# Performance work log

Hardware: AMD Instinct MI355X
Metric: run time of the kernel (lower is better)

## Reference

```python
import jax, jax.numpy as jnp
import numpy as np

D_MODEL, D_STATE, D_CONV, EXPAND = 1024, 16, 4, 2
D_INNER = EXPAND * D_MODEL
DT_RANK = (D_MODEL + 15) // 16  # 64
B_SZ, SEQ = 2, 1024


def _mamba_dir(x, inW, convW, convB, xpW, dtW, dtB, Alog, Dp, outW):
    """Standard Mamba block forward. x: [B, L, d_model]."""
    Bsz, L, _ = x.shape
    d_inner, d_state = Alog.shape
    dt_rank = xpW.shape[0] - 2 * d_state
    xz = jnp.einsum('bld,ed->ble', x, inW)            # [B, L, 2*d_inner]
    xi, z = jnp.split(xz, 2, axis=-1)
    # depthwise causal conv along L
    xc = jnp.swapaxes(xi, 1, 2)                       # [B, d_inner, L]
    xc = jax.lax.conv_general_dilated(
        xc, convW, window_strides=(1,),
        padding=[(convW.shape[-1] - 1, 0)],
        feature_group_count=d_inner)
    xc = xc + convB[None, :, None]
    u = jax.nn.silu(jnp.swapaxes(xc, 1, 2))           # [B, L, d_inner]
    x_dbl = jnp.einsum('bld,ed->ble', u, xpW)         # [B, L, dt_rank+2N]
    dt, Bm, Cm = jnp.split(x_dbl, [dt_rank, dt_rank + d_state], axis=-1)
    delta = jax.nn.softplus(jnp.einsum('blr,dr->bld', dt, dtW) + dtB)  # [B,L,d_inner]
    A = -jnp.exp(Alog)                                # [d_inner, d_state]

    def step(h, ins):
        d_t, B_t, C_t, u_t = ins                      # [B,D],[B,N],[B,N],[B,D]
        dA = jnp.exp(d_t[:, :, None] * A)             # [B, D, N]
        h = h * dA + (d_t * u_t)[:, :, None] * B_t[:, None, :]
        y_t = jnp.einsum('bdn,bn->bd', h, C_t)
        return h, y_t

    h0 = jnp.zeros((Bsz, d_inner, d_state), x.dtype)
    xs = (jnp.swapaxes(delta, 0, 1), jnp.swapaxes(Bm, 0, 1),
          jnp.swapaxes(Cm, 0, 1), jnp.swapaxes(u, 0, 1))
    _, ys = jax.lax.scan(step, h0, xs)
    y = jnp.swapaxes(ys, 0, 1)                        # [B, L, d_inner]
    y = y + u * Dp
    y = y * jax.nn.silu(z)
    return jnp.einsum('bld,od->blo', y, outW)         # [B, L, d_model]


def _make_params(key, suffix):
    ks = jax.random.split(key, 10)
    s = 0.02
    p = {
        'inW' + suffix: jax.random.normal(ks[0], (2 * D_INNER, D_MODEL), jnp.float32) * s,
        'convW' + suffix: jax.random.normal(ks[1], (D_INNER, 1, D_CONV), jnp.float32) * s,
        'convB' + suffix: jnp.zeros((D_INNER,), jnp.float32),
        'xpW' + suffix: jax.random.normal(ks[2], (DT_RANK + 2 * D_STATE, D_INNER), jnp.float32) * s,
        'dtW' + suffix: jax.random.normal(ks[3], (D_INNER, DT_RANK), jnp.float32) * s,
        'dtB' + suffix: jax.random.normal(ks[4], (D_INNER,), jnp.float32) * 0.1 - 4.0,
        'Alog' + suffix: jnp.log(1.0 + jax.random.uniform(ks[5], (D_INNER, D_STATE), jnp.float32) * 15.0),
        'Dp' + suffix: jnp.ones((D_INNER,), jnp.float32),
        'outW' + suffix: jax.random.normal(ks[6], (D_MODEL, D_INNER), jnp.float32) * s,
    }
    return p


def setup_inputs() -> dict:
    key = jax.random.key(0)
    kx, kf, kb = jax.random.split(key, 3)
    inp = {'x': jax.random.normal(kx, (B_SZ, SEQ, D_MODEL), jnp.float32)}
    inp.update(_make_params(kf, '_f'))
    inp.update(_make_params(kb, '_b'))
    return inp


def reference(x, inW_f, convW_f, convB_f, xpW_f, dtW_f, dtB_f, Alog_f, Dp_f, outW_f,
              inW_b, convW_b, convB_b, xpW_b, dtW_b, dtB_b, Alog_b, Dp_b, outW_b):
    y_fwd = _mamba_dir(x, inW_f, convW_f, convB_f, xpW_f, dtW_f, dtB_f, Alog_f, Dp_f, outW_f)
    xb = jnp.flip(x, axis=1)
    y_bwd = jnp.flip(_mamba_dir(xb, inW_b, convW_b, convB_b, xpW_b, dtW_b, dtB_b, Alog_b, Dp_b, outW_b), axis=1)
    return 0.5 * (y_fwd + y_bwd)
```

## Files before the change

kernel.cpp:

```cpp
#include <hip/hip_runtime.h>
#include <math.h>

#define B_SZ 2
#define SEQ  1024
#define DM   1024
#define DI   2048
#define NST  16
#define RNK  64
#define XPD  96
#define M_TOT (B_SZ*SEQ)
#define NC   32
#define LC   (SEQ/NC)
#define NCH  65536

typedef unsigned short ushort_t;
typedef __attribute__((ext_vector_type(8))) short short8;
typedef __attribute__((ext_vector_type(4))) float f32x4;

#if __has_builtin(__builtin_amdgcn_exp2f)
#define EXP2F __builtin_amdgcn_exp2f
#else
#define EXP2F exp2f
#endif
#define LOG2E 1.44269504f

__device__ __forceinline__ ushort_t f2bf(float f) {
    unsigned u = __float_as_uint(f);
    u += 0x7fff + ((u >> 16) & 1);
    return (ushort_t)(u >> 16);
}
__device__ __forceinline__ float bf2f(ushort_t v) {
    return __uint_as_float(((unsigned)v) << 16);
}

__global__ __launch_bounds__(256)
void convert_all(const float* __restrict__ x,
                 const float* __restrict__ inWf, const float* __restrict__ inWb,
                 const float* __restrict__ outWf, const float* __restrict__ outWb,
                 const float* __restrict__ xpWf, const float* __restrict__ xpWb,
                 ushort_t* __restrict__ xbf, ushort_t* __restrict__ inWcat,
                 ushort_t* __restrict__ outWcat, ushort_t* __restrict__ xpWcat)
{
    int bid = blockIdx.x;
    const float* src; ushort_t* dst; int rel; int strided = 0;
    if (bid < 2048)       { rel = bid;         src = x;     dst = xbf; }
    else if (bid < 6144)  { rel = bid - 2048;  src = inWf;  dst = inWcat; }
    else if (bid < 10240) { rel = bid - 6144;  src = inWb;  dst = inWcat + (size_t)2 * DI * DM; }
    else if (bid < 12288) { rel = bid - 10240; src = outWf; dst = outWcat;      strided = 1; }
    else if (bid < 14336) { rel = bid - 12288; src = outWb; dst = outWcat + DI; strided = 1; }
    else if (bid < 14528) { rel = bid - 14336; src = xpWf;  dst = xpWcat; }
    else                  { rel = bid - 14528; src = xpWb;  dst = xpWcat + (size_t)XPD * DI; }
    int i = rel * 256 + threadIdx.x;
    float4 v = ((const float4*)src)[i];
    ushort4 o;
    o.x = f2bf(v.x); o.y = f2bf(v.y); o.z = f2bf(v.z); o.w = f2bf(v.w);
    if (!strided) {
        ((ushort4*)dst)[i] = o;
    } else {
        int row = i >> 9;
        int c4  = (i - (row << 9)) << 2;
        *(ushort4*)(dst + (size_t)row * (2 * DI) + c4) = o;
    }
}

__device__ __forceinline__ void load_lds16(const ushort_t* g, ushort_t* l) {
    __builtin_amdgcn_global_load_lds(
        (const __attribute__((address_space(1))) void*)g,
        (__attribute__((address_space(3))) void*)l, 16, 0, 0);
}

template<bool OUT_BF16>
__global__ __launch_bounds__(256)
void gemm_gll(const ushort_t* __restrict__ A, const ushort_t* __restrict__ W,
              void* __restrict__ D, int M, int N, int K, int kLen, int ldD)
{
    __shared__ __align__(16) ushort_t As[128 * 64];
    __shared__ __align__(16) ushort_t Ws[128 * 64];
    const int t    = threadIdx.x;
    const int lane = t & 63;
    const int wave = t >> 6;
    const int wr   = (wave >> 1) * 64;
    const int wc   = (wave & 1) * 64;

    const int m0 = blockIdx.y * 128;
    const int n0 = blockIdx.x * 128;
    const int kStart = blockIdx.z * kLen;

    const int srow   = lane >> 3;
    const int gchunk = (lane & 7) ^ srow;

    f32x4 acc[4][4] = {};

    for (int k0 = kStart; k0 < kStart + kLen; k0 += 64) {
#pragma unroll
        for (int it = 0; it < 4; it++) {
            const int rb = wave * 32 + it * 8;
            load_lds16(A + (size_t)(m0 + rb + srow) * K + k0 + gchunk * 8,
                       As + rb * 64);
            load_lds16(W + (size_t)(n0 + rb + srow) * K + k0 + gchunk * 8,
                       Ws + rb * 64);
        }
        __syncthreads();
#pragma unroll
        for (int kk = 0; kk < 2; kk++) {
            const int kc = kk * 4 + (lane >> 4);
            short8 af[4], bf[4];
#pragma unroll
            for (int i = 0; i < 4; i++) {
                int r = wr + i * 16 + (lane & 15);
                af[i] = *(const short8*)(As + r * 64 + ((kc ^ (r & 7)) << 3));
            }
#pragma unroll
            for (int j = 0; j < 4; j++) {
                int r = wc + j * 16 + (lane & 15);
                bf[j] = *(const short8*)(Ws + r * 64 + ((kc ^ (r & 7)) << 3));
            }
#pragma unroll
            for (int i = 0; i < 4; i++)
#pragma unroll
                for (int j = 0; j < 4; j++)
                    acc[i][j] = __builtin_amdgcn_mfma_f32_16x16x32_bf16(
                        af[i], bf[j], acc[i][j], 0, 0, 0);
        }
        __syncthreads();
    }

    if (OUT_BF16) {
        ushort_t* Dp = (ushort_t*)D;
#pragma unroll
        for (int i = 0; i < 4; i++)
#pragma unroll
            for (int r = 0; r < 4; r++) {
                int m = m0 + wr + i * 16 + ((lane >> 4) << 2) + r;
#pragma unroll
                for (int j = 0; j < 4; j++) {
                    int n = n0 + wc + j * 16 + (lane & 15);
                    Dp[(size_t)m * ldD + n] = f2bf(acc[i][j][r]);
                }
            }
    } else {
        float* Dp = (float*)D + (size_t)blockIdx.z * M * ldD;
#pragma unroll
        for (int i = 0; i < 4; i++)
#pragma unroll
            for (int r = 0; r < 4; r++) {
                int m = m0 + wr + i * 16 + ((lane >> 4) << 2) + r;
#pragma unroll
                for (int j = 0; j < 4; j++) {
                    int n = n0 + wc + j * 16 + (lane & 15);
                    Dp[(size_t)m * ldD + n] = acc[i][j][r];
                }
            }
    }
}

__global__ __launch_bounds__(256)
void reduce4(const float* __restrict__ P, float* __restrict__ out)
{
    int i = blockIdx.x * 256 + threadIdx.x;
    const size_t S = (size_t)M_TOT * DM / 4;
    float4 a = ((const float4*)P)[i];
    float4 b = ((const float4*)P)[i + S];
    float4 c = ((const float4*)P)[i + 2 * S];
    float4 d = ((const float4*)P)[i + 3 * S];
    float4 o;
    o.x = 0.5f * (a.x + b.x + c.x + d.x);
    o.y = 0.5f * (a.y + b.y + c.y + d.y);
    o.z = 0.5f * (a.z + b.z + c.z + d.z);
    o.w = 0.5f * (a.w + b.w + c.w + d.w);
    ((float4*)out)[i] = o;
}

#define LDSP 72

__global__ __launch_bounds__(256)
void gemm2_splitk2(const ushort_t* __restrict__ ubf, const ushort_t* __restrict__ xpWcat,
                   float* __restrict__ P)
{
    const int dir = blockIdx.z >> 3;
    const int kz  = blockIdx.z & 7;
    const ushort_t* A = ubf + (size_t)dir * M_TOT * DI;
    const ushort_t* W = xpWcat + (size_t)dir * XPD * DI;
    const int K = DI, N = XPD;

    __shared__ __align__(16) ushort_t As[64 * LDSP];
    __shared__ __align__(16) ushort_t Ws[64 * LDSP];
    const int t    = threadIdx.x;
    const int lane = t & 63;
    const int wave = t >> 6;
    const int wr   = (wave >> 1) * 32;
    const int wc   = (wave & 1) * 32;

    f32x4 acc[2][2] = {};

    const int m0 = blockIdx.y * 64;
    const int n0 = blockIdx.x * 64;
    const int kStart = kz * (DI / 8);
    const int srow = t >> 3;
    const int scol = (t & 7) << 3;

    for (int k0 = kStart; k0 < kStart + DI / 8; k0 += 64) {
        {
            int r = srow;
            short8 v = *(const short8*)(A + (size_t)(m0 + r) * K + k0 + scol);
            *(short8*)(&As[r * LDSP + scol]) = v;
            int r2 = 32 + srow;
            short8 v2 = *(const short8*)(A + (size_t)(m0 + r2) * K + k0 + scol);
            *(short8*)(&As[r2 * LDSP + scol]) = v2;
            int wn = n0 + r;
            short8 wv = {};
            if (wn < N) wv = *(const short8*)(W + (size_t)wn * K + k0 + scol);
            *(short8*)(&Ws[r * LDSP + scol]) = wv;
            int wn2 = n0 + r2;
            short8 wv2 = {};
            if (wn2 < N) wv2 = *(const short8*)(W + (size_t)wn2 * K + k0 + scol);
            *(short8*)(&Ws[r2 * LDSP + scol]) = wv2;
        }
        __syncthreads();
#pragma unroll
        for (int kk = 0; kk < 2; kk++) {
            const int kcol = kk * 32 + ((lane >> 4) << 3);
            short8 af[2], bfr[2];
#pragma unroll
            for (int i = 0; i < 2; i++)
                af[i] = *(const short8*)(&As[(wr + i * 16 + (lane & 15)) * LDSP + kcol]);
#pragma unroll
            for (int j = 0; j < 2; j++)
                bfr[j] = *(const short8*)(&Ws[(wc + j * 16 + (lane & 15)) * LDSP + kcol]);
#pragma unroll
            for (int i = 0; i < 2; i++)
#pragma unroll
                for (int j = 0; j < 2; j++)
                    acc[i][j] = __builtin_amdgcn_mfma_f32_16x16x32_bf16(
                        af[i], bfr[j], acc[i][j], 0, 0, 0);
        }
        __syncthreads();
    }

    float* Pz = P + ((size_t)dir * 8 + kz) * M_TOT * XPD;
#pragma unroll
    for (int i = 0; i < 2; i++)
#pragma unroll
        for (int r = 0; r < 4; r++) {
            int m = m0 + wr + i * 16 + ((lane >> 4) << 2) + r;
#pragma unroll
            for (int j = 0; j < 2; j++) {
                int n = n0 + wc + j * 16 + (lane & 15);
                if (n < N) Pz[(size_t)m * XPD + n] = acc[i][j][r];
            }
        }
}

__global__ __launch_bounds__(256)
void xdbl_reduce2(const float* __restrict__ P, float* __restrict__ xdbl)
{
    int bid = blockIdx.x;
    int dir = bid >= 192;
    int i = (bid - dir * 192) * 256 + threadIdx.x;
    const size_t S = (size_t)M_TOT * XPD / 4;
    const float4* Pd = (const float4*)(P + (size_t)dir * 8 * M_TOT * XPD);
    float4 s = Pd[i];
#pragma unroll
    for (int z = 1; z < 8; z++) {
        float4 v = Pd[i + z * S];
        s.x += v.x; s.y += v.y; s.z += v.z; s.w += v.w;
    }
    ((float4*)(xdbl + (size_t)dir * M_TOT * XPD))[i] = s;
}

__global__ __launch_bounds__(256)
void delta_gemm2(const float* __restrict__ xdbl,
                 const float* __restrict__ dtWf, const float* __restrict__ dtWb,
                 const float* __restrict__ dtBf, const float* __restrict__ dtBb,
                 ushort_t* __restrict__ deltab)
{
    const int dir = blockIdx.z;
    const float* xd  = xdbl + (size_t)dir * M_TOT * XPD;
    const float* dtW = dir ? dtWb : dtWf;
    const float* dtB = dir ? dtBb : dtBf;
    ushort_t* delta  = deltab + (size_t)dir * M_TOT * DI;

    __shared__ __align__(16) ushort_t As[64 * LDSP];
    __shared__ __align__(16) ushort_t Ws[64 * LDSP];
    const int t    = threadIdx.x;
    const int lane = t & 63;
    const int wave = t >> 6;
    const int wr   = (wave >> 1) * 32;
    const int wc   = (wave & 1) * 32;

    const int m0 = blockIdx.y * 64;
    const int n0 = blockIdx.x * 64;
    const int srow = t >> 2;
    const int scol = (t & 3) << 4;

    {
        const float* ap = xd  + (size_t)(m0 + srow) * XPD + scol;
        const float* wp = dtW + (size_t)(n0 + srow) * RNK + scol;
        float4 a[4], w[4];
#pragma unroll
        for (int q = 0; q < 4; q++) { a[q] = ((const float4*)ap)[q]; w[q] = ((const float4*)wp)[q]; }
        __align__(16) ushort_t at[16], wt[16];
#pragma unroll
        for (int q = 0; q < 16; q++) {
            at[q] = f2bf(((const float*)a)[q]);
            wt[q] = f2bf(((const float*)w)[q]);
        }
        *(short8*)(&As[srow * LDSP + scol])     = *(const short8*)(at);
        *(short8*)(&As[srow * LDSP + scol + 8]) = *(const short8*)(at + 8);
        *(short8*)(&Ws[srow * LDSP + scol])     = *(const short8*)(wt);
        *(short8*)(&Ws[srow * LDSP + scol + 8]) = *(const short8*)(wt + 8);
    }
    __syncthreads();

    f32x4 acc[2][2] = {};
#pragma unroll
    for (int kk = 0; kk < 2; kk++) {
        const int kcol = kk * 32 + ((lane >> 4) << 3);
        short8 af[2], bfr[2];
#pragma unroll
        for (int i = 0; i < 2; i++)
            af[i] = *(const short8*)(&As[(wr + i * 16 + (lane & 15)) * LDSP + kcol]);
#pragma unroll
        for (int j = 0; j < 2; j++)
            bfr[j] = *(const short8*)(&Ws[(wc + j * 16 + (lane & 15)) * LDSP + kcol]);
#pragma unroll
        for (int i = 0; i < 2; i++)
#pragma unroll
            for (int j = 0; j < 2; j++)
                acc[i][j] = __builtin_amdgcn_mfma_f32_16x16x32_bf16(
                    af[i], bfr[j], acc[i][j], 0, 0, 0);
    }

#pragma unroll
    for (int j = 0; j < 2; j++) {
        int n = n0 + wc + j * 16 + (lane & 15);
        float bn = dtB[n];
#pragma unroll
        for (int i = 0; i < 2; i++) {
#pragma unroll
            for (int r = 0; r < 4; r++) {
                int m = m0 + wr + i * 16 + ((lane >> 4) << 2) + r;
                float v = acc[i][j][r] + bn;
                float sp = (v > 20.f) ? v : log1pf(__expf(v));
                delta[(size_t)m * DI + n] = f2bf(sp);
            }
        }
    }
}

__global__ __launch_bounds__(256)
void conv_silu2(const ushort_t* __restrict__ xzall,
                const float* __restrict__ convWf, const float* __restrict__ convWb,
                const float* __restrict__ convBf, const float* __restrict__ convBb,
                ushort_t* __restrict__ ubf)
{
    int bid = blockIdx.x;
    int dir = bid >> 12;
    int idx = (bid & 4095) * 256 + threadIdx.x;
    const float* convW = dir ? convWb : convWf;
    const float* convB = dir ? convBb : convBf;
    int di  = (idx & (DI / 4 - 1)) << 2;
    int m   = idx >> 9;
    int b   = m >> 10, l = m & (SEQ - 1);
    const ushort_t* xb = xzall + (size_t)b * SEQ * (4 * DI) + dir * (2 * DI) + di;

    float wv[4][4];
#pragma unroll
    for (int c = 0; c < 4; c++) {
        float4 w = *(const float4*)(convW + (di + c) * 4);
        wv[c][0] = w.x; wv[c][1] = w.y; wv[c][2] = w.z; wv[c][3] = w.w;
    }
    float4 cb = *(const float4*)(convB + di);
    float acc[4] = {cb.x, cb.y, cb.z, cb.w};
#pragma unroll
    for (int j = 0; j < 4; j++) {
        int srcl = dir ? (l + 3 - j) : (l - 3 + j);
        if ((unsigned)srcl < SEQ) {
            ushort4 xv = *(const ushort4*)(xb + (size_t)srcl * (4 * DI));
            acc[0] += wv[0][j] * bf2f(xv.x);
            acc[1] += wv[1][j] * bf2f(xv.y);
            acc[2] += wv[2][j] * bf2f(xv.z);
            acc[3] += wv[3][j] * bf2f(xv.w);
        }
    }
    ushort4 o;
    o.x = f2bf(acc[0] / (1.f + __expf(-acc[0])));
    o.y = f2bf(acc[1] / (1.f + __expf(-acc[1])));
    o.z = f2bf(acc[2] / (1.f + __expf(-acc[2])));
    o.w = f2bf(acc[3] / (1.f + __expf(-acc[3])));
    *(ushort4*)(ubf + (size_t)dir * M_TOT * DI + (size_t)m * DI + di) = o;
}

__global__ __launch_bounds__(256)
void scan_pass1_2(const ushort_t* __restrict__ deltab, const ushort_t* __restrict__ ubf,
                  const float* __restrict__ xdbl,
                  const float* __restrict__ Alogf, const float* __restrict__ Alogb,
                  float* __restrict__ Sb, float* __restrict__ SD)
{
    int tid = threadIdx.x, lane = tid & 63, wv = tid >> 6;
    int blk = blockIdx.x;
    int dir = blk >> 9;
    blk &= 511;
    int dg = blk & 7;
    int bc = blk >> 3;
    int c  = bc & (NC - 1);
    int b  = bc >> 5;
    int d  = (dg * 4 + wv) * 64 + lane;
    int t0 = dir ? (SEQ - 1 - c * LC) : (c * LC);
    int rs = dir ? -1 : 1;

    const float* Alog = dir ? Alogb : Alogf;
    const ushort_t* dl_p = deltab + (size_t)dir * M_TOT * DI;
    const ushort_t* u_p  = ubf    + (size_t)dir * M_TOT * DI;
    const float*    xd   = xdbl   + (size_t)dir * M_TOT * XPD;
    float* Sbd = Sb + (size_t)dir * NC * NCH;
    float* SDd = SD + (size_t)dir * NC * B_SZ * DI;

    float ac2[NST];
#pragma unroll
    for (int q = 0; q < 4; q++) {
        float4 al = *(const float4*)(Alog + (size_t)d * NST + q * 4);
        ac2[q * 4 + 0] = -__expf(al.x) * LOG2E;
        ac2[q * 4 + 1] = -__expf(al.y) * LOG2E;
        ac2[q * 4 + 2] = -__expf(al.z) * LOG2E;
        ac2[q * 4 + 3] = -__expf(al.w) * LOG2E;
    }
    float h[NST];
#pragma unroll
    for (int n = 0; n < NST; n++) h[n] = 0.f;
    float sumD = 0.f;

#pragma unroll 4
    for (int l = 0; l < LC; l++) {
        int t = t0 + rs * l;
        size_t row = (size_t)b * SEQ + t;
        float dl = bf2f(dl_p[row * DI + d]);
        float uv = bf2f(u_p[row * DI + d]);
        const float* xr = xd + row * XPD + RNK;
        float4 Bv[4];
#pragma unroll
        for (int q = 0; q < 4; q++) Bv[q] = *(const float4*)(xr + q * 4);
        float dlu = dl * uv;
        sumD += dl;
#pragma unroll
        for (int n = 0; n < NST; n++) {
            float dA = EXP2F(dl * ac2[n]);
            h[n] = h[n] * dA + dlu * ((const float*)Bv)[n];
        }
    }

    size_t o = (size_t)c * NCH + ((size_t)b * DI + d) * NST;
#pragma unroll
    for (int q = 0; q < 4; q++)
        *(float4*)(Sbd + o + q * 4) = make_float4(h[q*4], h[q*4+1], h[q*4+2], h[q*4+3]);
    SDd[(size_t)c * (B_SZ * DI) + b * DI + d] = sumD;
}

__global__ __launch_bounds__(256)
void scan_combine2(float* __restrict__ Sb, const float* __restrict__ SD,
                   const float* __restrict__ Alogf, const float* __restrict__ Alogb)
{
    int gid = blockIdx.x * 256 + threadIdx.x;
    int dir = gid >= NCH;
    int i = gid - dir * NCH;
    int n = i & 15;
    int d = (i >> 4) & (DI - 1);
    int b = i >> 15;
    const float* Alog = dir ? Alogb : Alogf;
    float* Sbd = Sb + (size_t)dir * NC * NCH;
    const float* SDd = SD + (size_t)dir * NC * B_SZ * DI;
    float ac2 = -__expf(Alog[(size_t)d * NST + n]) * LOG2E;
    float h = 0.f;
#pragma unroll
    for (int c = 0; c < NC; c++) {
        float s = Sbd[(size_t)c * NCH + i];
        float p = EXP2F(ac2 * SDd[(size_t)c * (B_SZ * DI) + b * DI + d]);
        Sbd[(size_t)c * NCH + i] = h;
        h = s + p * h;
    }
}

__global__ __launch_bounds__(256)
void scan_pass2_2(const ushort_t* __restrict__ deltab, const ushort_t* __restrict__ ubf,
                  const float* __restrict__ xdbl, const ushort_t* __restrict__ xzall,
                  const float* __restrict__ Alogf, const float* __restrict__ Alogb,
                  const float* __restrict__ Dpf, const float* __restrict__ Dpb,
                  const float* __restrict__ Hinit, ushort_t* __restrict__ ybf)
{
    int tid = threadIdx.x, lane = tid & 63, wv = tid >> 6;
    int blk = blockIdx.x;
    int dir = blk >> 9;
    blk &= 511;
    int dg = blk & 7;
    int bc = blk >> 3;
    int c  = bc & (NC - 1);
    int b  = bc >> 5;
    int d  = (dg * 4 + wv) * 64 + lane;
    int t0 = dir ? (SEQ - 1 - c * LC) : (c * LC);
    int rs = dir ? -1 : 1;

    const float* Alog = dir ? Alogb : Alogf;
    const float* Dpp  = dir ? Dpb : Dpf;
    const ushort_t* dl_p = deltab + (size_t)dir * M_TOT * DI;
    const ushort_t* u_p  = ubf    + (size_t)dir * M_TOT * DI;
    const float*    xd   = xdbl   + (size_t)dir * M_TOT * XPD;
    const float*    Hin  = Hinit  + (size_t)dir * NC * NCH;

    float ac2[NST];
#pragma unroll
    for (int q = 0; q < 4; q++) {
        float4 al = *(const float4*)(Alog + (size_t)d * NST + q * 4);
        ac2[q * 4 + 0] = -__expf(al.x) * LOG2E;
        ac2[q * 4 + 1] = -__expf(al.y) * LOG2E;
        ac2[q * 4 + 2] = -__expf(al.z) * LOG2E;
        ac2[q * 4 + 3] = -__expf(al.w) * LOG2E;
    }
    float dp = Dpp[d];
    float h[NST];
    {
        size_t o = (size_t)c * NCH + ((size_t)b * DI + d) * NST;
#pragma unroll
        for (int q = 0; q < 4; q++) {
            float4 hv = *(const float4*)(Hin + o + q * 4);
            h[q*4] = hv.x; h[q*4+1] = hv.y; h[q*4+2] = hv.z; h[q*4+3] = hv.w;
        }
    }

#pragma unroll 4
    for (int l = 0; l < LC; l++) {
        int t = t0 + rs * l;
        size_t row = (size_t)b * SEQ + t;
        float dl = bf2f(dl_p[row * DI + d]);
        float uv = bf2f(u_p[row * DI + d]);
        const float* xr = xd + row * XPD + RNK;
        float4 Bv[4], Cv[4];
#pragma unroll
        for (int q = 0; q < 4; q++) {
            Bv[q] = *(const float4*)(xr + q * 4);
            Cv[q] = *(const float4*)(xr + NST + q * 4);
        }
        float dlu = dl * uv;
        float y = 0.f;
#pragma unroll
        for (int n = 0; n < NST; n++) {
            float dA = EXP2F(dl * ac2[n]);
            h[n] = h[n] * dA + dlu * ((const float*)Bv)[n];
            y += h[n] * ((const float*)Cv)[n];
        }
        float z = bf2f(xzall[row * (4 * DI) + dir * (2 * DI) + DI + d]);
        float yv = (y + uv * dp) * (z / (1.f + __expf(-z)));
        ybf[row * (2 * DI) + dir * DI + d] = f2bf(yv);
    }
}

extern "C" void kernel_launch(void* const* d_in, const int* in_sizes, int n_in,
                              void* d_out, int out_size, void* d_ws, size_t ws_size,
                              hipStream_t stream)
{
    char* wsb = (char*)d_ws;

    ushort_t* xzall  = (ushort_t*)wsb;
    ushort_t* ybf    = (ushort_t*)(wsb + 33554432);
    ushort_t* inWcat = (ushort_t*)(wsb + 50331648);
    ushort_t* outWcat= (ushort_t*)(wsb + 67108864);
    ushort_t* xbf    = (ushort_t*)(wsb + 75497472);
    ushort_t* xpWcat = (ushort_t*)(wsb + 79691776);
    ushort_t* ubf    = (ushort_t*)(wsb + 80478208);
    ushort_t* deltab = (ushort_t*)(wsb + 97255424);
    float*    xdbl   = (float*)(wsb + 114032640);

    float* Sb    = (float*)inWcat;
    float* SD    = (float*)xbf;
    float* part2 = (float*)deltab;
    float* part4 = (float*)xzall;

    float* out = (float*)d_out;
    dim3 blk(256);

    convert_all<<<14720, blk, 0, stream>>>(
        (const float*)d_in[0], (const float*)d_in[1], (const float*)d_in[10],
        (const float*)d_in[9], (const float*)d_in[18],
        (const float*)d_in[4], (const float*)d_in[13],
        xbf, inWcat, outWcat, xpWcat);

    gemm_gll<true><<<dim3(8192 / 128, M_TOT / 128, 1), blk, 0, stream>>>(
        xbf, inWcat, xzall, M_TOT, 8192, DM, DM, 8192);

    conv_silu2<<<8192, blk, 0, stream>>>(xzall,
        (const float*)d_in[2], (const float*)d_in[11],
        (const float*)d_in[3], (const float*)d_in[12], ubf);

    gemm2_splitk2<<<dim3(2, M_TOT / 64, 16), blk, 0, stream>>>(ubf, xpWcat, part2);

    xdbl_reduce2<<<384, blk, 0, stream>>>(part2, xdbl);

    delta_gemm2<<<dim3(DI / 64, M_TOT / 64, 2), blk, 0, stream>>>(
        xdbl, (const float*)d_in[5], (const float*)d_in[14],
        (const float*)d_in[6], (const float*)d_in[15], deltab);

    scan_pass1_2<<<1024, blk, 0, stream>>>(deltab, ubf, xdbl,
        (const float*)d_in[7], (const float*)d_in[16], Sb, SD);
    scan_combine2<<<2 * NCH / 256, blk, 0, stream>>>(Sb, SD,
        (const float*)d_in[7], (const float*)d_in[16]);
    scan_pass2_2<<<1024, blk, 0, stream>>>(deltab, ubf, xdbl, xzall,
        (const float*)d_in[7], (const float*)d_in[16],
        (const float*)d_in[8], (const float*)d_in[17], Sb, ybf);

    gemm_gll<false><<<dim3(DM / 128, M_TOT / 128, 4), blk, 0, stream>>>(
        ybf, outWcat, part4, M_TOT, DM, 2 * DI, DI / 2, DM);

    reduce4<<<(M_TOT * DM / 4) / 256, blk, 0, stream>>>(part4, out);
}
```

Measured before the change: 358.4 us.

## Replace input projection GEMM with 256x256 double-buffered 8-wave bf16 MFMA kernel

Adds a new bf16 GEMM kernel with 256x256 output tiles, 512 threads and double-buffered LDS staging via global_load_lds. The K loop is split into four quarter-steps, each interleaving async loads, barriers and MFMA bursts with raised wave priority. It is used for the large input projection GEMM (2048x8192x1024) in place of the 128x128 kernel. Larger tiles raise data reuse per LDS load and overlap memory with compute. The cost is heavy LDS use (128 KB per block), only 256 blocks, and many barriers per iteration.

```diff
diff --git a/kernel.cpp b/kernel.cpp
--- a/kernel.cpp
+++ b/kernel.cpp
@@ -69,6 +69,149 @@
         (__attribute__((address_space(3))) void*)l, 16, 0, 0);
 }
 
+__device__ __forceinline__ void stageHalf(const ushort_t* g, int grow0, int K, int kt,
+                                          ushort_t* lds, int w8, int l8, int gch)
+{
+    const ushort_t* p = g + (size_t)(grow0 + w8 + l8) * K + (size_t)kt * 64 + (gch << 3);
+    load_lds16(p,                  lds + w8 * 64);
+    load_lds16(p + (size_t)64 * K, lds + (64 + w8) * 64);
+}
+
+__device__ __forceinline__ void rdA4(const ushort_t* buf, int rbase, int sw0, int sw1,
+                                     short8 (&a)[4][2])
+{
+#pragma unroll
+    for (int i = 0; i < 4; i++) {
+        const ushort_t* p = buf + (size_t)(rbase + i * 16) * 64;
+        a[i][0] = *(const short8*)(p + sw0);
+        a[i][1] = *(const short8*)(p + sw1);
+    }
+}
+__device__ __forceinline__ void rdB2(const ushort_t* buf, int rbase, int sw0, int sw1,
+                                     short8 (&bb)[2][2])
+{
+#pragma unroll
+    for (int j = 0; j < 2; j++) {
+        const ushort_t* p = buf + (size_t)(rbase + j * 16) * 64;
+        bb[j][0] = *(const short8*)(p + sw0);
+        bb[j][1] = *(const short8*)(p + sw1);
+    }
+}
+__device__ __forceinline__ void mm16(const short8 (&a)[4][2], const short8 (&bb)[2][2],
+                                     f32x4 (&acc)[4][2])
+{
+#pragma unroll
+    for (int i = 0; i < 4; i++)
+#pragma unroll
+        for (int j = 0; j < 2; j++) {
+            acc[i][j] = __builtin_amdgcn_mfma_f32_16x16x32_bf16(a[i][0], bb[j][0], acc[i][j], 0, 0, 0);
+            acc[i][j] = __builtin_amdgcn_mfma_f32_16x16x32_bf16(a[i][1], bb[j][1], acc[i][j], 0, 0, 0);
+        }
+}
+
+#define BAR()        __builtin_amdgcn_s_barrier()
+#define SCHEDB()     __builtin_amdgcn_sched_barrier(0)
+#define PRIO1()      __builtin_amdgcn_s_setprio(1)
+#define PRIO0()      __builtin_amdgcn_s_setprio(0)
+#define WAIT_LGKM0() asm volatile("s_waitcnt lgkmcnt(0)" ::: "memory")
+#define WAIT_VM6()   asm volatile("s_waitcnt vmcnt(6)"  ::: "memory")
+#define WAIT_VM0()   asm volatile("s_waitcnt vmcnt(0)"  ::: "memory")
+
+__global__ __launch_bounds__(512, 2)
+void gemm256_bf16(const ushort_t* __restrict__ A, const ushort_t* __restrict__ W,
+                  ushort_t* __restrict__ D, int K, int ldD)
+{
+    __shared__ __align__(16) ushort_t As[2][256 * 64];
+    __shared__ __align__(16) ushort_t Bs[2][256 * 64];
+
+    const int t_   = threadIdx.x;
+    const int lane = t_ & 63;
+    const int wave = t_ >> 6;
+    const int wrq  = wave >> 2;
+    const int wcq  = wave & 3;
+    const int lm   = lane & 15;
+    const int w8   = wave << 3;
+    const int l8   = lane >> 3;
+    const int gch  = (lane & 7) ^ l8;
+    const int sw0  = (((lane >> 4)    ) ^ (lane & 7)) << 3;
+    const int sw1  = (((lane >> 4) + 4) ^ (lane & 7)) << 3;
+
+    const int m0 = blockIdx.y * 256;
+    const int n0 = blockIdx.x * 256;
+    const int NT = K >> 6;
+
+    const int rA0 = wrq * 64 + lm, rA1 = 128 + rA0;
+    const int rB0 = wcq * 32 + lm, rB1 = 128 + rB0;
+
+    f32x4 acc[2][2][4][2] = {};
+    short8 a[4][2], b0[2][2], b1[2][2];
+
+    stageHalf(A, m0,       K, 0, &As[0][0],        w8, l8, gch);
+    stageHalf(A, m0 + 128, K, 0, &As[0][128 * 64], w8, l8, gch);
+    stageHalf(W, n0,       K, 0, &Bs[0][0],        w8, l8, gch);
+    stageHalf(W, n0 + 128, K, 0, &Bs[0][128 * 64], w8, l8, gch);
+    if (NT > 1) {
+        stageHalf(A, m0,       K, 1, &As[1][0],        w8, l8, gch);
+        stageHalf(W, n0,       K, 1, &Bs[1][0],        w8, l8, gch);
+        stageHalf(W, n0 + 128, K, 1, &Bs[1][128 * 64], w8, l8, gch);
+        WAIT_VM6();
+    } else {
+        WAIT_VM0();
+    }
+    BAR();
+
+    for (int t = 0; t < NT; ++t) {
+        const int b = t & 1;
+        const ushort_t* Ab = &As[b][0];
+        const ushort_t* Bb = &Bs[b][0];
+        ushort_t* Abw = &As[b][0];
+        ushort_t* Bbw = &Bs[b][0];
+        ushort_t* Aow = &As[b ^ 1][0];
+
+        rdA4(Ab, rA0, sw0, sw1, a);
+        rdB2(Bb, rB0, sw0, sw1, b0);
+        if (t + 1 < NT) stageHalf(A, m0 + 128, K, t + 1, Aow + 128 * 64, w8, l8, gch);
+        SCHEDB(); BAR(); WAIT_LGKM0(); SCHEDB();
+        PRIO1(); mm16(a, b0, acc[0][0]); PRIO0();
+        SCHEDB(); BAR();
+
+        rdB2(Bb, rB1, sw0, sw1, b1);
+        if (t + 2 < NT) stageHalf(A, m0, K, t + 2, Abw, w8, l8, gch);
+        SCHEDB(); BAR(); WAIT_LGKM0(); SCHEDB();
+        PRIO1(); mm16(a, b1, acc[0][1]); PRIO0();
+        SCHEDB(); BAR();
+
+        rdA4(Ab, rA1, sw0, sw1, a);
+        if (t + 2 < NT) stageHalf(W, n0, K, t + 2, Bbw, w8, l8, gch);
+        SCHEDB(); BAR(); WAIT_LGKM0(); SCHEDB();
+        PRIO1(); mm16(a, b1, acc[1][1]); PRIO0();
+        SCHEDB(); BAR();
+
+        if (t + 2 < NT) stageHalf(W, n0 + 128, K, t + 2, Bbw + 128 * 64, w8, l8, gch);
+        SCHEDB(); BAR();
+        PRIO1(); mm16(a, b0, acc[1][0]); PRIO0();
+        SCHEDB();
+        if (t < NT - 2) { WAIT_VM6(); } else { WAIT_VM0(); }
+        BAR();
+    }
+
+#pragma unroll
+    for (int ih = 0; ih < 2; ih++)
+#pragma unroll
+        for (int i = 0; i < 4; i++)
+#pragma unroll
+            for (int r = 0; r < 4; r++) {
+                int m = m0 + ih * 128 + wrq * 64 + i * 16 + ((lane >> 4) << 2) + r;
+#pragma unroll
+                for (int jh = 0; jh < 2; jh++)
+#pragma unroll
+                    for (int j = 0; j < 2; j++) {
+                        int n = n0 + jh * 128 + wcq * 32 + j * 16 + lm;
+                        D[(size_t)m * ldD + n] = f2bf(acc[ih][jh][i][j][r]);
+                    }
+            }
+}
+
 template<bool OUT_BF16>
 __global__ __launch_bounds__(256)
 void gemm_gll(const ushort_t* __restrict__ A, const ushort_t* __restrict__ W,
@@ -583,8 +726,8 @@
         (const float*)d_in[4], (const float*)d_in[13],
         xbf, inWcat, outWcat, xpWcat);
 
-    gemm_gll<true><<<dim3(8192 / 128, M_TOT / 128, 1), blk, 0, stream>>>(
-        xbf, inWcat, xzall, M_TOT, 8192, DM, DM, 8192);
+    gemm256_bf16<<<dim3(8192 / 256, M_TOT / 256), dim3(512), 0, stream>>>(
+        xbf, inWcat, xzall, DM, 8192);
 
     conv_silu2<<<8192, blk, 0, stream>>>(xzall,
         (const float*)d_in[2], (const float*)d_in[11],
```

After: 348.9 us. 2.6% less time.
